# Kernel optimization log

Hardware: AMD Instinct MI355X
Metric: run time of the kernel (lower is better)

## Reference

```python
import jax, jax.numpy as jnp
import numpy as np

NUM_ITERS = 10  # forward() runs power_iteration with num_iters=10


def setup_inputs() -> dict:
    key = jax.random.key(0)
    k1, k2 = jax.random.split(key)
    out_ch, in_ch, h, w = 2048, 2048, 3, 3
    conv_filter = jax.random.normal(k1, (out_ch, in_ch, h, w), dtype=jnp.float32) * 0.02
    u = jax.random.normal(k2, (1, in_ch * w), dtype=jnp.float32)
    u = u / jnp.linalg.norm(u, axis=1, keepdims=True)
    return {"conv_filter": conv_filter, "u": u}


def reference(conv_filter, u):
    out_ch, in_ch, h, w = conv_filter.shape
    # permute (0,2,1,3) then view as [out_ch*h, in_ch*w]
    W = jnp.transpose(conv_filter, (0, 2, 1, 3)).reshape(out_ch * h, in_ch * w)
    Ws = jax.lax.stop_gradient(W)  # power iteration vectors are detached

    def body(i, carry):
        u_n, _ = carry
        v = u_n @ Ws.T                                   # [1, out_ch*h]
        v_n = v / jnp.linalg.norm(v, axis=1, keepdims=True)
        u2 = v_n @ Ws                                    # [1, in_ch*w]
        u_n2 = u2 / jnp.linalg.norm(u2, axis=1, keepdims=True)
        return (u_n2, v_n)

    v0 = jnp.zeros((1, out_ch * h), dtype=conv_filter.dtype)  # overwritten in first iter
    u_n, v_n = jax.lax.fori_loop(0, NUM_ITERS, body, (u, v0))

    # sigma = v W u^T with u, v treated as constants (custom autograd Function)
    sigma = (v_n @ W) @ u_n.T                            # [1, 1]
    return jnp.sqrt(jnp.asarray(h * w, dtype=conv_filter.dtype)) * sigma
```

## Files before the change

### kernel.cpp

```cpp
#include <hip/hip_runtime.h>
#include <hip/hip_bf16.h>
#include <hip/hip_fp16.h>

#define OC_N     2048
#define IC_N     2048
#define RC       6144
#define OCSTRIDE 18432
#define UNSCALE  0.0000152587890625f

typedef float v2f __attribute__((ext_vector_type(2)));

__device__ __forceinline__ float wave_reduce(float x) {
#pragma unroll
    for (int off = 32; off > 0; off >>= 1) x += __shfl_down(x, off, 64);
    return x;
}

__global__ __launch_bounds__(256) void convert_q_kernel(
    const float* __restrict__ conv, unsigned char* __restrict__ Wq)
{
    const int t  = blockIdx.x * 256 + threadIdx.x;
    const int o8 = t * 8;
    const int r  = o8 / RC;
    const int c0 = o8 % RC;
    const int oc = r / 3, hh = r % 3;
    const float* base = conv + (size_t)oc * OCSTRIDE + hh * 3;
    float f[8];
#pragma unroll
    for (int e = 0; e < 8; ++e) {
        const int c  = c0 + e;
        const int ic = c / 3, ww = c - 3 * ic;
        f[e] = base[ic * 9 + ww] * 256.0f;
    }
    int lo = __builtin_amdgcn_cvt_pk_fp8_f32(f[0], f[1], 0, false);
    lo     = __builtin_amdgcn_cvt_pk_fp8_f32(f[2], f[3], lo, true);
    int hi = __builtin_amdgcn_cvt_pk_fp8_f32(f[4], f[5], 0, false);
    hi     = __builtin_amdgcn_cvt_pk_fp8_f32(f[6], f[7], hi, true);
    *reinterpret_cast<uint2*>(Wq + o8) = make_uint2((unsigned)lo, (unsigned)hi);
}

__global__ __launch_bounds__(256) void transpose_q_kernel(
    const unsigned char* __restrict__ Wq, unsigned char* __restrict__ WqT)
{
    __shared__ unsigned char tile[64][68];
    const int tid = threadIdx.x;
    const int tr  = blockIdx.x;
    const int tc  = blockIdx.y;

    const int r  = tid >> 2;
    const int cq = (tid & 3) * 16;
    const uint4 w = *reinterpret_cast<const uint4*>(
        Wq + (size_t)(tr * 64 + r) * RC + tc * 64 + cq);
    *reinterpret_cast<unsigned int*>(&tile[r][cq +  0]) = w.x;
    *reinterpret_cast<unsigned int*>(&tile[r][cq +  4]) = w.y;
    *reinterpret_cast<unsigned int*>(&tile[r][cq +  8]) = w.z;
    *reinterpret_cast<unsigned int*>(&tile[r][cq + 12]) = w.w;
    __syncthreads();

    const int orow = tid >> 2;
    const int ocq  = (tid & 3) * 16;
    unsigned int u32s[4];
#pragma unroll
    for (int wi = 0; wi < 4; ++wi) {
        const int ro = ocq + 4 * wi;
        u32s[wi] =  (unsigned int)tile[ro + 0][orow]
                 | ((unsigned int)tile[ro + 1][orow] << 8)
                 | ((unsigned int)tile[ro + 2][orow] << 16)
                 | ((unsigned int)tile[ro + 3][orow] << 24);
    }
    uint4 o = make_uint4(u32s[0], u32s[1], u32s[2], u32s[3]);
    *reinterpret_cast<uint4*>(WqT + (size_t)(tc * 64 + orow) * RC + tr * 64 + ocq) = o;
}

__device__ __forceinline__ float dot16(uint4 w, float4 a, float4 b, float4 c, float4 d) {
    float acc = 0.f;
    v2f f;
    f = __builtin_amdgcn_cvt_pk_f32_fp8(w.x, false); acc += f.x * a.x + f.y * a.y;
    f = __builtin_amdgcn_cvt_pk_f32_fp8(w.x, true);  acc += f.x * a.z + f.y * a.w;
    f = __builtin_amdgcn_cvt_pk_f32_fp8(w.y, false); acc += f.x * b.x + f.y * b.y;
    f = __builtin_amdgcn_cvt_pk_f32_fp8(w.y, true);  acc += f.x * b.z + f.y * b.w;
    f = __builtin_amdgcn_cvt_pk_f32_fp8(w.z, false); acc += f.x * c.x + f.y * c.y;
    f = __builtin_amdgcn_cvt_pk_f32_fp8(w.z, true);  acc += f.x * c.z + f.y * c.w;
    f = __builtin_amdgcn_cvt_pk_f32_fp8(w.w, false); acc += f.x * d.x + f.y * d.y;
    f = __builtin_amdgcn_cvt_pk_f32_fp8(w.w, true);  acc += f.x * d.z + f.y * d.w;
    return acc;
}

__global__ __launch_bounds__(256) void matvec_q_kernel(
    const unsigned char* __restrict__ W, const float* __restrict__ x,
    float* __restrict__ y, float scale)
{
    __shared__ float x_lds[7680];
    float4* x4 = reinterpret_cast<float4*>(x_lds);

    const int tid  = threadIdx.x;
    const int lane = tid & 63;
    const int wid  = tid >> 6;

    const float4* s4 = reinterpret_cast<const float4*>(x);
#pragma unroll
    for (int k = 0; k < 6; ++k) {
        const int g = tid + 256 * k;
        x4[g + (g >> 2)] = s4[g];
    }
    __syncthreads();

    const int rbase = blockIdx.x * 8 + wid * 2;
    const unsigned char* w0 = W + (size_t)rbase * RC;
    float acc0 = 0.f, acc1 = 0.f;
#pragma unroll
    for (int i = 0; i < 6; ++i) {
        const int slot = i * 320 + lane * 5;
        const float4 a = x4[slot + 0];
        const float4 b = x4[slot + 1];
        const float4 c = x4[slot + 2];
        const float4 d = x4[slot + 3];
        const uint4 wA = *reinterpret_cast<const uint4*>(w0 +      i * 1024 + lane * 16);
        const uint4 wB = *reinterpret_cast<const uint4*>(w0 + RC + i * 1024 + lane * 16);
        acc0 += dot16(wA, a, b, c, d);
        acc1 += dot16(wB, a, b, c, d);
    }
    acc0 = wave_reduce(acc0);
    acc1 = wave_reduce(acc1);
    if (lane == 0) { y[rbase] = acc0 * scale; y[rbase + 1] = acc1 * scale; }
}

__global__ __launch_bounds__(256) void vstep_kernel(
    const float* __restrict__ conv, const float* __restrict__ u,
    float* __restrict__ v_out)
{
    __shared__ float u_lds[RC];
    __shared__ float sred[8];
    __shared__ float sred3[12];
    __shared__ float sbcast;

    const int tid  = threadIdx.x;
    const int oc   = blockIdx.x;
    const int lane = tid & 63;
    const int wid  = tid >> 6;

    float sq = 0.f;
    const float4* u4  = reinterpret_cast<const float4*>(u);
    float4*       ul4 = reinterpret_cast<float4*>(u_lds);
#pragma unroll
    for (int k = 0; k < 6; ++k) {
        float4 q = u4[tid + 256 * k];
        ul4[tid + 256 * k] = q;
        sq += q.x * q.x + q.y * q.y + q.z * q.z + q.w * q.w;
    }
    float wsum = wave_reduce(sq);
    if (lane == 0) sred[wid] = wsum;
    __syncthreads();
    if (tid == 0) sbcast = rsqrtf(sred[0] + sred[1] + sred[2] + sred[3]);
    __syncthreads();
    const float scale = sbcast;

    float acc0 = 0.f, acc1 = 0.f, acc2 = 0.f;
    const float* base = conv + (size_t)oc * OCSTRIDE;
#pragma unroll
    for (int gi = 0; gi < 2; ++gi) {
        const int g = tid + 256 * gi;
        const float4* p4  = reinterpret_cast<const float4*>(base + g * 36);
        const float4* q12 = reinterpret_cast<const float4*>(u_lds + 12 * g);
        float uv[12];
#pragma unroll
        for (int k = 0; k < 3; ++k) {
            float4 q = q12[k];
            uv[4 * k] = q.x; uv[4 * k + 1] = q.y; uv[4 * k + 2] = q.z; uv[4 * k + 3] = q.w;
        }
#pragma unroll
        for (int j = 0; j < 9; ++j) {
            float4 q = p4[j];
            float el[4] = {q.x, q.y, q.z, q.w};
#pragma unroll
            for (int e = 0; e < 4; ++e) {
                const int m   = 4 * j + e;
                const int icl = m / 9;
                const int rem = m - 9 * icl;
                const int hh  = rem / 3;
                const int ww  = rem - 3 * hh;
                const float pv = el[e] * uv[icl * 3 + ww];
                if (hh == 0) acc0 += pv;
                else if (hh == 1) acc1 += pv;
                else acc2 += pv;
            }
        }
    }
    acc0 = wave_reduce(acc0);
    acc1 = wave_reduce(acc1);
    acc2 = wave_reduce(acc2);
    if (lane == 0) { sred3[wid] = acc0; sred3[4 + wid] = acc1; sred3[8 + wid] = acc2; }
    __syncthreads();
    if (tid < 3) {
        const float s = sred3[tid * 4 + 0] + sred3[tid * 4 + 1] +
                        sred3[tid * 4 + 2] + sred3[tid * 4 + 3];
        v_out[oc * 3 + tid] = scale * s;
    }
}

__global__ __launch_bounds__(256) void final_kernel(
    const float* __restrict__ v, const float* __restrict__ t,
    float* __restrict__ out)
{
    __shared__ float ssq[4];
    __shared__ float sdot[4];
    const int tid  = threadIdx.x;
    const int lane = tid & 63;
    const int wid  = tid >> 6;
    float sq = 0.f, dot = 0.f;
#pragma unroll
    for (int k = 0; k < 24; ++k) {
        float x = v[tid + 256 * k];
        float y = t[tid + 256 * k];
        sq  += x * x;
        dot += x * y;
    }
    sq  = wave_reduce(sq);
    dot = wave_reduce(dot);
    if (lane == 0) { ssq[wid] = sq; sdot[wid] = dot; }
    __syncthreads();
    if (tid == 0) {
        const float sqt  = ssq[0] + ssq[1] + ssq[2] + ssq[3];
        const float dott = sdot[0] + sdot[1] + sdot[2] + sdot[3];
        out[0] = 3.0f * dott * rsqrtf(sqt);
    }
}

extern "C" void kernel_launch(void* const* d_in, const int* in_sizes, int n_in,
                              void* d_out, int out_size, void* d_ws, size_t ws_size,
                              hipStream_t stream)
{
    const float* conv = (const float*)d_in[0];
    const float* u_in = (const float*)d_in[1];
    float* out = (float*)d_out;

    const size_t WQ_BYTES = (size_t)RC * RC;
    const size_t needed = 2 * WQ_BYTES + (size_t)3 * RC * sizeof(float);
    if (ws_size < needed) return;

    unsigned char* Wq  = (unsigned char*)d_ws;
    unsigned char* WqT = Wq + WQ_BYTES;
    float* v_vec = (float*)(WqT + WQ_BYTES);
    float* u_vec = v_vec + RC;
    float* t_vec = u_vec + RC;

    convert_q_kernel<<<RC * RC / 8 / 256, 256, 0, stream>>>(conv, Wq);
    transpose_q_kernel<<<dim3(RC / 64, RC / 64), 256, 0, stream>>>(Wq, WqT);

    for (int i = 0; i < 10; ++i) {
        matvec_q_kernel<<<RC / 8, 256, 0, stream>>>(
            Wq, (i == 0) ? u_in : u_vec, v_vec, 1.0f);
        matvec_q_kernel<<<RC / 8, 256, 0, stream>>>(
            WqT, v_vec, u_vec, UNSCALE);
    }

    vstep_kernel<<<OC_N, 256, 0, stream>>>(conv, u_vec, t_vec);
    final_kernel<<<1, 256, 0, stream>>>(v_vec, t_vec, out);
}
```

Measured before the change: 423.0 us.

## Fuse power-iteration matvec launches into one persistent kernel with grid barriers

Replaces the 20 separate matvec kernel launches with one persistent kernel of 768 blocks. The blocks synchronise between matvec phases through a flag-based software grid barrier held in workspace memory, and the flags are zeroed inside the convert kernel. The aim is to remove per-launch overhead and launch gaps between the small matvecs. In exchange it relies on all 768 blocks being co-resident (launch_bounds of 3 blocks per CU), otherwise the barrier deadlocks, and the barrier adds spin-wait cost to every phase.

```diff
diff --git a/kernel.cpp b/kernel.cpp
--- a/kernel.cpp
+++ b/kernel.cpp
@@ -7,6 +7,7 @@
 #define RC       6144
 #define OCSTRIDE 18432
 #define UNSCALE  0.0000152587890625f
+#define NBLK     768
 
 typedef float v2f __attribute__((ext_vector_type(2)));
 
@@ -17,8 +18,12 @@
 }
 
 __global__ __launch_bounds__(256) void convert_q_kernel(
-    const float* __restrict__ conv, unsigned char* __restrict__ Wq)
-{
+    const float* __restrict__ conv, unsigned char* __restrict__ Wq,
+    int* __restrict__ flags)
+{
+    if (blockIdx.x == 0) {
+        for (int k = threadIdx.x; k < NBLK + 1; k += 256) flags[k] = 0;
+    }
     const int t  = blockIdx.x * 256 + threadIdx.x;
     const int o8 = t * 8;
     const int r  = o8 / RC;
@@ -86,26 +91,20 @@
     return acc;
 }
 
-__global__ __launch_bounds__(256) void matvec_q_kernel(
-    const unsigned char* __restrict__ W, const float* __restrict__ x,
-    float* __restrict__ y, float scale)
-{
-    __shared__ float x_lds[7680];
-    float4* x4 = reinterpret_cast<float4*>(x_lds);
-
-    const int tid  = threadIdx.x;
-    const int lane = tid & 63;
-    const int wid  = tid >> 6;
-
+__device__ __forceinline__ void stage_x(const float* __restrict__ x,
+                                        float4* __restrict__ x4, int tid) {
     const float4* s4 = reinterpret_cast<const float4*>(x);
 #pragma unroll
     for (int k = 0; k < 6; ++k) {
         const int g = tid + 256 * k;
         x4[g + (g >> 2)] = s4[g];
     }
-    __syncthreads();
-
-    const int rbase = blockIdx.x * 8 + wid * 2;
+}
+
+__device__ __forceinline__ void matvec_rows2(
+    const unsigned char* __restrict__ W, const float4* __restrict__ x4,
+    int rbase, int lane, float* out0, float* out1)
+{
     const unsigned char* w0 = W + (size_t)rbase * RC;
     float acc0 = 0.f, acc1 = 0.f;
 #pragma unroll
@@ -120,9 +119,71 @@
         acc0 += dot16(wA, a, b, c, d);
         acc1 += dot16(wB, a, b, c, d);
     }
-    acc0 = wave_reduce(acc0);
-    acc1 = wave_reduce(acc1);
-    if (lane == 0) { y[rbase] = acc0 * scale; y[rbase + 1] = acc1 * scale; }
+    *out0 = wave_reduce(acc0);
+    *out1 = wave_reduce(acc1);
+}
+
+__device__ __forceinline__ void grid_barrier(int* __restrict__ flags,
+                                             int* __restrict__ gen,
+                                             int bid, int tid, int g)
+{
+    __syncthreads();
+    if (tid == 0) {
+        __threadfence();
+        __hip_atomic_store(&flags[bid], g, __ATOMIC_RELAXED, __HIP_MEMORY_SCOPE_AGENT);
+    }
+    if (bid == 0 && tid < 64) {
+        const int base = tid * 12;
+        for (;;) {
+            bool ok = true;
+#pragma unroll
+            for (int k = 0; k < 12; ++k)
+                ok &= (__hip_atomic_load(&flags[base + k], __ATOMIC_RELAXED,
+                                         __HIP_MEMORY_SCOPE_AGENT) >= g);
+            if (__all(ok)) break;
+            __builtin_amdgcn_s_sleep(1);
+        }
+        if (tid == 0)
+            __hip_atomic_store(gen, g, __ATOMIC_RELAXED, __HIP_MEMORY_SCOPE_AGENT);
+    }
+    if (tid == 0) {
+        while (__hip_atomic_load(gen, __ATOMIC_RELAXED, __HIP_MEMORY_SCOPE_AGENT) < g)
+            __builtin_amdgcn_s_sleep(1);
+        __builtin_amdgcn_fence(__ATOMIC_ACQUIRE, "agent");
+    }
+    __syncthreads();
+}
+
+__global__ __launch_bounds__(256, 3) void power_iter_kernel(
+    const unsigned char* __restrict__ Wq, const unsigned char* __restrict__ WqT,
+    const float* __restrict__ u_in, float* __restrict__ u_vec,
+    float* __restrict__ v_vec, int* __restrict__ flags)
+{
+    __shared__ float x_lds[7680];
+    float4* x4 = reinterpret_cast<float4*>(x_lds);
+    int* gen = flags + NBLK;
+
+    const int tid   = threadIdx.x;
+    const int lane  = tid & 63;
+    const int wid   = tid >> 6;
+    const int bid   = blockIdx.x;
+    const int rbase = bid * 8 + wid * 2;
+    int g = 0;
+
+    for (int it = 0; it < 10; ++it) {
+        stage_x(it == 0 ? u_in : u_vec, x4, tid);
+        __syncthreads();
+        float a0, a1;
+        matvec_rows2(Wq, x4, rbase, lane, &a0, &a1);
+        if (lane == 0) { v_vec[rbase] = a0; v_vec[rbase + 1] = a1; }
+        ++g; grid_barrier(flags, gen, bid, tid, g);
+
+        stage_x(v_vec, x4, tid);
+        __syncthreads();
+        matvec_rows2(WqT, x4, rbase, lane, &a0, &a1);
+        if (lane == 0) { u_vec[rbase] = a0 * UNSCALE; u_vec[rbase + 1] = a1 * UNSCALE; }
+        if (it != 9) { ++g; grid_barrier(flags, gen, bid, tid, g); }
+    }
 }
 
 __global__ __launch_bounds__(256) void vstep_kernel(
@@ -235,7 +296,8 @@
     float* out = (float*)d_out;
 
     const size_t WQ_BYTES = (size_t)RC * RC;
-    const size_t needed = 2 * WQ_BYTES + (size_t)3 * RC * sizeof(float);
+    const size_t needed = 2 * WQ_BYTES + (size_t)3 * RC * sizeof(float)
+                        + (NBLK + 1) * sizeof(int);
     if (ws_size < needed) return;
 
     unsigned char* Wq  = (unsigned char*)d_ws;
@@ -243,16 +305,11 @@
     float* v_vec = (float*)(WqT + WQ_BYTES);
     float* u_vec = v_vec + RC;
     float* t_vec = u_vec + RC;
-
-    convert_q_kernel<<<RC * RC / 8 / 256, 256, 0, stream>>>(conv, Wq);
+    int*   flags = (int*)(t_vec + RC);
+
+    convert_q_kernel<<<RC * RC / 8 / 256, 256, 0, stream>>>(conv, Wq, flags);
     transpose_q_kernel<<<dim3(RC / 64, RC / 64), 256, 0, stream>>>(Wq, WqT);
-
-    for (int i = 0; i < 10; ++i) {
-        matvec_q_kernel<<<RC / 8, 256, 0, stream>>>(
-            Wq, (i == 0) ? u_in : u_vec, v_vec, 1.0f);
-        matvec_q_kernel<<<RC / 8, 256, 0, stream>>>(
-            WqT, v_vec, u_vec, UNSCALE);
-    }
+    power_iter_kernel<<<NBLK, 256, 0, stream>>>(Wq, WqT, u_in, u_vec, v_vec, flags);
 
     vstep_kernel<<<OC_N, 256, 0, stream>>>(conv, u_vec, t_vec);
     final_kernel<<<1, 256, 0, stream>>>(v_vec, t_vec, out);
```

New measurement: 1.495 ms. 3.53x slower.

## Drop fp32 final pass and LDS staging; compute sigma from FP8 matvec

Applied to the files above, without the earlier changes.

Replaces the final full-precision vstep pass over the fp32 conv filter with another FP8 matvec over the quantized weight, and folds u normalisation and the quantization unscale into the final reduction. The matvec kernel no longer stages x in LDS and now computes one row per wave, with twice as many blocks. This removes a large fp32 weight read at the end and the LDS barrier. In exchange the final sigma now comes from quantized weights, which lowers accuracy, and x is re-read from global/L2 by every wave.

```diff
diff --git a/kernel.cpp b/kernel.cpp
--- a/kernel.cpp
+++ b/kernel.cpp
@@ -90,139 +90,58 @@
     const unsigned char* __restrict__ W, const float* __restrict__ x,
     float* __restrict__ y, float scale)
 {
-    __shared__ float x_lds[7680];
-    float4* x4 = reinterpret_cast<float4*>(x_lds);
-
     const int tid  = threadIdx.x;
     const int lane = tid & 63;
     const int wid  = tid >> 6;
+    const int r    = blockIdx.x * 4 + wid;
 
-    const float4* s4 = reinterpret_cast<const float4*>(x);
-#pragma unroll
-    for (int k = 0; k < 6; ++k) {
-        const int g = tid + 256 * k;
-        x4[g + (g >> 2)] = s4[g];
-    }
-    __syncthreads();
-
-    const int rbase = blockIdx.x * 8 + wid * 2;
-    const unsigned char* w0 = W + (size_t)rbase * RC;
-    float acc0 = 0.f, acc1 = 0.f;
+    const unsigned char* w0 = W + (size_t)r * RC;
+    const float4* x4 = reinterpret_cast<const float4*>(x);
+    float acc = 0.f;
 #pragma unroll
     for (int i = 0; i < 6; ++i) {
-        const int slot = i * 320 + lane * 5;
-        const float4 a = x4[slot + 0];
-        const float4 b = x4[slot + 1];
-        const float4 c = x4[slot + 2];
-        const float4 d = x4[slot + 3];
-        const uint4 wA = *reinterpret_cast<const uint4*>(w0 +      i * 1024 + lane * 16);
-        const uint4 wB = *reinterpret_cast<const uint4*>(w0 + RC + i * 1024 + lane * 16);
-        acc0 += dot16(wA, a, b, c, d);
-        acc1 += dot16(wB, a, b, c, d);
+        const int c = i * 1024 + lane * 16;
+        const uint4 w = *reinterpret_cast<const uint4*>(w0 + c);
+        const float4 a = x4[(c >> 2) + 0];
+        const float4 b = x4[(c >> 2) + 1];
+        const float4 e = x4[(c >> 2) + 2];
+        const float4 d = x4[(c >> 2) + 3];
+        acc += dot16(w, a, b, e, d);
     }
-    acc0 = wave_reduce(acc0);
-    acc1 = wave_reduce(acc1);
-    if (lane == 0) { y[rbase] = acc0 * scale; y[rbase + 1] = acc1 * scale; }
-}
-
-__global__ __launch_bounds__(256) void vstep_kernel(
-    const float* __restrict__ conv, const float* __restrict__ u,
-    float* __restrict__ v_out)
-{
-    __shared__ float u_lds[RC];
-    __shared__ float sred[8];
-    __shared__ float sred3[12];
-    __shared__ float sbcast;
-
-    const int tid  = threadIdx.x;
-    const int oc   = blockIdx.x;
-    const int lane = tid & 63;
-    const int wid  = tid >> 6;
-
-    float sq = 0.f;
-    const float4* u4  = reinterpret_cast<const float4*>(u);
-    float4*       ul4 = reinterpret_cast<float4*>(u_lds);
-#pragma unroll
-    for (int k = 0; k < 6; ++k) {
-        float4 q = u4[tid + 256 * k];
-        ul4[tid + 256 * k] = q;
-        sq += q.x * q.x + q.y * q.y + q.z * q.z + q.w * q.w;
-    }
-    float wsum = wave_reduce(sq);
-    if (lane == 0) sred[wid] = wsum;
-    __syncthreads();
-    if (tid == 0) sbcast = rsqrtf(sred[0] + sred[1] + sred[2] + sred[3]);
-    __syncthreads();
-    const float scale = sbcast;
-
-    float acc0 = 0.f, acc1 = 0.f, acc2 = 0.f;
-    const float* base = conv + (size_t)oc * OCSTRIDE;
-#pragma unroll
-    for (int gi = 0; gi < 2; ++gi) {
-        const int g = tid + 256 * gi;
-        const float4* p4  = reinterpret_cast<const float4*>(base + g * 36);
-        const float4* q12 = reinterpret_cast<const float4*>(u_lds + 12 * g);
-        float uv[12];
-#pragma unroll
-        for (int k = 0; k < 3; ++k) {
-            float4 q = q12[k];
-            uv[4 * k] = q.x; uv[4 * k + 1] = q.y; uv[4 * k + 2] = q.z; uv[4 * k + 3] = q.w;
-        }
-#pragma unroll
-        for (int j = 0; j < 9; ++j) {
-            float4 q = p4[j];
-            float el[4] = {q.x, q.y, q.z, q.w};
-#pragma unroll
-            for (int e = 0; e < 4; ++e) {
-                const int m   = 4 * j + e;
-                const int icl = m / 9;
-                const int rem = m - 9 * icl;
-                const int hh  = rem / 3;
-                const int ww  = rem - 3 * hh;
-                const float pv = el[e] * uv[icl * 3 + ww];
-                if (hh == 0) acc0 += pv;
-                else if (hh == 1) acc1 += pv;
-                else acc2 += pv;
-            }
-        }
-    }
-    acc0 = wave_reduce(acc0);
-    acc1 = wave_reduce(acc1);
-    acc2 = wave_reduce(acc2);
-    if (lane == 0) { sred3[wid] = acc0; sred3[4 + wid] = acc1; sred3[8 + wid] = acc2; }
-    __syncthreads();
-    if (tid < 3) {
-        const float s = sred3[tid * 4 + 0] + sred3[tid * 4 + 1] +
-                        sred3[tid * 4 + 2] + sred3[tid * 4 + 3];
-        v_out[oc * 3 + tid] = scale * s;
-    }
+    acc = wave_reduce(acc);
+    if (lane == 0) y[r] = acc * scale;
 }
 
 __global__ __launch_bounds__(256) void final_kernel(
     const float* __restrict__ v, const float* __restrict__ t,
-    float* __restrict__ out)
+    const float* __restrict__ u, float* __restrict__ out)
 {
-    __shared__ float ssq[4];
+    __shared__ float ssv[4];
+    __shared__ float ssu[4];
     __shared__ float sdot[4];
     const int tid  = threadIdx.x;
     const int lane = tid & 63;
     const int wid  = tid >> 6;
-    float sq = 0.f, dot = 0.f;
+    float sqv = 0.f, squ = 0.f, dot = 0.f;
 #pragma unroll
     for (int k = 0; k < 24; ++k) {
-        float x = v[tid + 256 * k];
-        float y = t[tid + 256 * k];
-        sq  += x * x;
-        dot += x * y;
+        const float xv = v[tid + 256 * k];
+        const float xt = t[tid + 256 * k];
+        const float xu = u[tid + 256 * k];
+        sqv += xv * xv;
+        squ += xu * xu;
+        dot += xv * xt;
     }
-    sq  = wave_reduce(sq);
+    sqv = wave_reduce(sqv);
+    squ = wave_reduce(squ);
     dot = wave_reduce(dot);
-    if (lane == 0) { ssq[wid] = sq; sdot[wid] = dot; }
+    if (lane == 0) { ssv[wid] = sqv; ssu[wid] = squ; sdot[wid] = dot; }
     __syncthreads();
     if (tid == 0) {
-        const float sqt  = ssq[0] + ssq[1] + ssq[2] + ssq[3];
-        const float dott = sdot[0] + sdot[1] + sdot[2] + sdot[3];
-        out[0] = 3.0f * dott * rsqrtf(sqt);
+        const float vs = ssv[0] + ssv[1] + ssv[2] + ssv[3];
+        const float us = ssu[0] + ssu[1] + ssu[2] + ssu[3];
+        const float dt = sdot[0] + sdot[1] + sdot[2] + sdot[3];
+        out[0] = (3.0f / 256.0f) * dt * rsqrtf(vs) * rsqrtf(us);
     }
 }
 
@@ -248,12 +167,12 @@
     transpose_q_kernel<<<dim3(RC / 64, RC / 64), 256, 0, stream>>>(Wq, WqT);
 
     for (int i = 0; i < 10; ++i) {
-        matvec_q_kernel<<<RC / 8, 256, 0, stream>>>(
+        matvec_q_kernel<<<RC / 4, 256, 0, stream>>>(
             Wq, (i == 0) ? u_in : u_vec, v_vec, 1.0f);
-        matvec_q_kernel<<<RC / 8, 256, 0, stream>>>(
+        matvec_q_kernel<<<RC / 4, 256, 0, stream>>>(
             WqT, v_vec, u_vec, UNSCALE);
     }
 
-    vstep_kernel<<<OC_N, 256, 0, stream>>>(conv, u_vec, t_vec);
-    final_kernel<<<1, 256, 0, stream>>>(v_vec, t_vec, out);
+    matvec_q_kernel<<<RC / 4, 256, 0, stream>>>(Wq, u_vec, t_vec, 1.0f);
+    final_kernel<<<1, 256, 0, stream>>>(v_vec, t_vec, u_vec, out);
 }
```

Result: slower. 479.5 us (+13.3%).
